# Kernel tuning notes

Measured on AMD Instinct MI355X. Metric: run time of the kernel, lower is better.

The kernel has to match this reference:

```python
import jax, jax.numpy as jnp
import numpy as np

BN_EPS = 1e-5


def setup_inputs() -> dict:
    key = jax.random.key(0)
    ks = jax.random.split(key, 12)
    B, C, L, P = 8, 128, 4096, 96
    d = C // 8
    return {
        "x": jax.random.normal(ks[0], (B, C, 1), jnp.float32),
        "Wt": jax.random.normal(ks[1], (C, C, L), jnp.float32) * 0.02,
        "bt": jax.random.normal(ks[2], (C,), jnp.float32) * 0.02,
        "gamma": jnp.ones((C,), jnp.float32),
        "beta": jnp.zeros((C,), jnp.float32),
        "Wq": jax.random.normal(ks[3], (d, C), jnp.float32) * 0.05,
        "bq": jax.random.normal(ks[4], (d,), jnp.float32) * 0.02,
        "Wk": jax.random.normal(ks[5], (d, C), jnp.float32) * 0.05,
        "bk": jax.random.normal(ks[6], (d,), jnp.float32) * 0.02,
        "Wv": jax.random.normal(ks[7], (C, C), jnp.float32) * 0.05,
        "bv": jax.random.normal(ks[8], (C,), jnp.float32) * 0.02,
        "W2": jax.random.normal(ks[9], (P, C), jnp.float32) * 0.05,
        "b2": jax.random.normal(ks[10], (P,), jnp.float32) * 0.02,
    }


def reference(x, Wt, bt, gamma, beta, Wq, bq, Wk, bk, Wv, bv, W2, b2):
    # l1: ConvTranspose1d(C, C, kernel=L, stride=1) on input of length 1
    # out[b, o, l] = sum_i x[b, i, 0] * Wt[i, o, l] + bt[o]
    h = jnp.einsum('bi,iol->bol', x[:, :, 0], Wt) + bt[None, :, None]  # [B,C,L]
    # BatchNorm1d (training mode: batch stats, biased variance)
    mean = jnp.mean(h, axis=(0, 2), keepdims=True)
    var = jnp.mean((h - mean) ** 2, axis=(0, 2), keepdims=True)
    h = (h - mean) * jax.lax.rsqrt(var + BN_EPS)
    h = h * gamma[None, :, None] + beta[None, :, None]
    h = jax.nn.relu(h)
    # Self_Attn: 1x1 conv projections
    q = jnp.einsum('qc,bcl->bql', Wq, h) + bq[None, :, None]   # [B,d,L]
    k = jnp.einsum('qc,bcl->bql', Wk, h) + bk[None, :, None]   # [B,d,L]
    v = jnp.einsum('oc,bcl->bol', Wv, h) + bv[None, :, None]   # [B,C,L]
    energy = jnp.einsum('bdl,bdm->blm', q, k)                  # [B,L,L]
    attn = jax.nn.softmax(energy, axis=-1)
    out = jnp.einsum('bcm,blm->bcl', v, attn)                  # [B,C,L]
    # l2: Conv1d(C -> P, kernel=1)
    y = jnp.einsum('pc,bcl->bpl', W2, out) + b2[None, :, None]  # [B,P,L]
    return y
```

## Files before the change

### kernel.cpp

```cpp
#include <hip/hip_runtime.h>

#define B_ 8
#define C_ 128
#define L_ 4096
#define P_ 96
#define D_ 16

typedef __attribute__((ext_vector_type(8))) short short8;
typedef __attribute__((ext_vector_type(16))) float float16v;

__device__ __forceinline__ unsigned short f2bf(float f) {
  unsigned int u = __float_as_uint(f);
  u += 0x7fff + ((u >> 16) & 1);
  return (unsigned short)(u >> 16);
}

constexpr size_t OFF_H      = 0;
constexpr size_t OFF_PSUM   = 16777216;
constexpr size_t OFF_PSUMSQ = OFF_PSUM + 8192;
constexpr size_t OFF_SCALE  = OFF_PSUMSQ + 8192;
constexpr size_t OFF_SHIFT  = OFF_SCALE + 512;
constexpr size_t OFF_WALLT  = OFF_SHIFT + 512;
constexpr size_t OFF_BALL   = OFF_WALLT + 65536;
constexpr size_t OFF_QT     = OFF_BALL + 512;
constexpr size_t OFF_KT     = OFF_QT + 1048576;
constexpr size_t OFF_V2     = OFF_KT + 1048576;

__global__ __launch_bounds__(128) void k_prep(
    const float* __restrict__ Wq, const float* __restrict__ bq,
    const float* __restrict__ Wk, const float* __restrict__ bk,
    const float* __restrict__ Wv, const float* __restrict__ bv,
    const float* __restrict__ W2,
    float* __restrict__ wallT, float* __restrict__ ball)
{
  const int r = blockIdx.x;
  const int c = threadIdx.x;
  float wv;
  if (r < 16) {
    wv = Wq[r * C_ + c];
  } else if (r < 32) {
    wv = Wk[(r - 16) * C_ + c];
  } else {
    const int p = r - 32;
    float s = 0.f;
#pragma unroll 8
    for (int o = 0; o < C_; ++o) s += W2[p * C_ + o] * Wv[o * C_ + c];
    wv = s;
  }
  wallT[c * C_ + r] = wv;
  if (c == 0) {
    float bb;
    if (r < 16)      bb = bq[r];
    else if (r < 32) bb = bk[r - 16];
    else {
      const int p = r - 32;
      float s = 0.f;
#pragma unroll 8
      for (int o = 0; o < C_; ++o) s += W2[p * C_ + o] * bv[o];
      bb = s;
    }
    ball[r] = bb;
  }
}

__global__ __launch_bounds__(512) void k_conv(
    const float* __restrict__ x, const float* __restrict__ Wt,
    float* __restrict__ h, float* __restrict__ psum, float* __restrict__ psumsq)
{
  __shared__ float4 xs4[256];
  __shared__ float rs1[8], rs2[8];
  const int tid = threadIdx.x;
  const int o = blockIdx.y;
  const int l = blockIdx.x * 2048 + tid * 4;

  if (tid < 256) xs4[tid] = ((const float4*)x)[tid];
  __syncthreads();

  float4 acc[8];
#pragma unroll
  for (int bb = 0; bb < 8; ++bb) acc[bb] = (float4){0.f, 0.f, 0.f, 0.f};

  const float* wp = Wt + (size_t)o * L_ + l;
  const size_t stride = (size_t)C_ * L_;
  const int phase = (blockIdx.y + blockIdx.x * 8) & 31;

  float4 wbuf[2][4];
#pragma unroll
  for (int q = 0; q < 4; ++q)
    wbuf[0][q] = *(const float4*)(wp + (size_t)(phase * 4 + q) * stride);

#pragma unroll 2
  for (int g = 0; g < 32; ++g) {
    const int cur = g & 1, nb = cur ^ 1;
    const int in4 = ((phase + g + 1) & 31) * 4;
#pragma unroll
    for (int q = 0; q < 4; ++q)
      wbuf[nb][q] = *(const float4*)(wp + (size_t)(in4 + q) * stride);

    const int ic = (phase + g) & 31;
#pragma unroll
    for (int bb = 0; bb < 8; ++bb) {
      const float4 xb = xs4[bb * 32 + ic];
      acc[bb].x += xb.x * wbuf[cur][0].x + xb.y * wbuf[cur][1].x + xb.z * wbuf[cur][2].x + xb.w * wbuf[cur][3].x;
      acc[bb].y += xb.x * wbuf[cur][0].y + xb.y * wbuf[cur][1].y + xb.z * wbuf[cur][2].y + xb.w * wbuf[cur][3].y;
      acc[bb].z += xb.x * wbuf[cur][0].z + xb.y * wbuf[cur][1].z + xb.z * wbuf[cur][2].z + xb.w * wbuf[cur][3].z;
      acc[bb].w += xb.x * wbuf[cur][0].w + xb.y * wbuf[cur][1].w + xb.z * wbuf[cur][2].w + xb.w * wbuf[cur][3].w;
    }
  }
  float s1 = 0.f, s2 = 0.f;
#pragma unroll
  for (int bb = 0; bb < 8; ++bb) {
    *(float4*)(h + ((size_t)(bb * C_ + o)) * L_ + l) = acc[bb];
    s1 += acc[bb].x + acc[bb].y + acc[bb].z + acc[bb].w;
    s2 += acc[bb].x * acc[bb].x + acc[bb].y * acc[bb].y
        + acc[bb].z * acc[bb].z + acc[bb].w * acc[bb].w;
  }
  for (int off = 1; off < 64; off <<= 1) {
    s1 += __shfl_xor(s1, off);
    s2 += __shfl_xor(s2, off);
  }
  if ((tid & 63) == 0) { rs1[tid >> 6] = s1; rs2[tid >> 6] = s2; }
  __syncthreads();
  if (tid == 0) {
    float a1 = 0.f, a2 = 0.f;
#pragma unroll
    for (int wv = 0; wv < 8; ++wv) { a1 += rs1[wv]; a2 += rs2[wv]; }
    psum[o * 2 + blockIdx.x]   = a1;
    psumsq[o * 2 + blockIdx.x] = a2;
  }
}

__global__ __launch_bounds__(128) void k_bn(
    const float* __restrict__ psum, const float* __restrict__ psumsq,
    const float* __restrict__ gamma, const float* __restrict__ beta,
    float* __restrict__ scale, float* __restrict__ shift)
{
  const int c = threadIdx.x;
  float s1 = 0.f, s2 = 0.f;
  for (int t = 0; t < 2; ++t) { s1 += psum[c * 2 + t]; s2 += psumsq[c * 2 + t]; }
  const float inv = 1.f / 32768.f;
  const float mean = s1 * inv;
  const float var  = s2 * inv - mean * mean;
  const float sc   = rsqrtf(var + 1e-5f) * gamma[c];
  scale[c] = sc;
  shift[c] = beta[c] - mean * sc;
}

__global__ __launch_bounds__(256) void k_proj(
    const float* __restrict__ h, const float* __restrict__ scale,
    const float* __restrict__ shift, const float* __restrict__ wallT,
    const float* __restrict__ ball,
    unsigned short* __restrict__ qT, unsigned short* __restrict__ kT,
    unsigned short* __restrict__ v2t)
{
  __shared__ __align__(16) char sm[128 * 68 * 4];
  float* hn = (float*)sm;
  unsigned short* v2s = (unsigned short*)sm;

  const int b = blockIdx.y;
  const int l0 = blockIdx.x * 64;
  const int tid = threadIdx.x;

#pragma unroll
  for (int i = 0; i < 8; ++i) {
    const int idx = tid + i * 256;
    const int c = idx >> 4, lq = (idx & 15) * 4;
    const float4 hv = *(const float4*)(h + ((size_t)(b * C_ + c)) * L_ + l0 + lq);
    const float sc = scale[c], sh = shift[c];
    float4 r;
    r.x = fmaxf(hv.x * sc + sh, 0.f);
    r.y = fmaxf(hv.y * sc + sh, 0.f);
    r.z = fmaxf(hv.z * sc + sh, 0.f);
    r.w = fmaxf(hv.w * sc + sh, 0.f);
    *(float4*)(hn + c * 68 + lq) = r;
  }
  __syncthreads();

  const int wu = __builtin_amdgcn_readfirstlane(tid) >> 6;
  const int lane = tid & 63;
  const int l = l0 + lane;

  float acc[32];
#pragma unroll
  for (int r = 0; r < 32; ++r) acc[r] = ball[wu * 32 + r];

#pragma unroll 4
  for (int c = 0; c < C_; ++c) {
    const float hv = hn[c * 68 + lane];
    const float* wrow = wallT + c * C_ + wu * 32;
#pragma unroll
    for (int r = 0; r < 32; ++r) acc[r] += wrow[r] * hv;
  }
  __syncthreads();

  if (wu == 0) {
    const size_t row = (size_t)(b * L_ + l) * D_;
    short8 v0, v1;
#pragma unroll
    for (int r = 0; r < 8; ++r) {
      v0[r] = (short)f2bf(acc[r] * 1.44269504f);
      v1[r] = (short)f2bf(acc[8 + r] * 1.44269504f);
    }
    *(short8*)(qT + row) = v0;  *(short8*)(qT + row + 8) = v1;
#pragma unroll
    for (int r = 0; r < 8; ++r) { v0[r] = (short)f2bf(acc[16 + r]); v1[r] = (short)f2bf(acc[24 + r]); }
    *(short8*)(kT + row) = v0;  *(short8*)(kT + row + 8) = v1;
  } else {
    const int pbase = wu * 32 - 32;
#pragma unroll
    for (int r = 0; r < 32; ++r)
      v2s[(pbase + r) * 72 + lane] = f2bf(acc[r]);
  }
  __syncthreads();

#pragma unroll
  for (int i = 0; i < 6; ++i) {
    const int j = tid + i * 256;
    const int mo4 = j & 3;
    const int jp = j >> 2;
    const int p = jp % 96;
    const int mtl = jp / 96;
    const uint2 val = *(const uint2*)(v2s + p * 72 + mtl * 16 + mo4 * 4);
    *(uint2*)(v2t + ((size_t)((b * (L_ / 16) + blockIdx.x * 4 + mtl)) * P_ + p) * 16
              + mo4 * 4) = val;
  }
}

__global__ __launch_bounds__(1024, 4) void k_attn(
    const unsigned short* __restrict__ qT, const unsigned short* __restrict__ kT,
    const unsigned short* __restrict__ v2t, const float* __restrict__ b2,
    float* __restrict__ y)
{
  __shared__ float ldsO[P_ * 128];
  __shared__ float ldsL[128];

  const int b = blockIdx.y;
  const int l0 = blockIdx.x * 128;
  const int tid = threadIdx.x;
  const int w  = tid >> 6;
  const int qg = w & 3;
  const int ms = w >> 2;
  const int lane = tid & 63;
  const int col = lane & 31;
  const int hh  = lane >> 5;

#pragma unroll
  for (int i = 0; i < 12; ++i) ldsO[tid + i * 1024] = 0.f;
  if (tid < 128) ldsL[tid] = 0.f;
  __syncthreads();

  const int lq = l0 + qg * 32 + col;
  const short8 qf = *(const short8*)(qT + ((size_t)(b * L_ + lq)) * D_ + hh * 8);

  float16v oacc[3];
#pragma unroll
  for (int pt = 0; pt < 3; ++pt)
#pragma unroll
    for (int r = 0; r < 16; ++r) oacc[pt][r] = 0.f;
  float lsum = 0.f;

  const unsigned short* kbase =
      kT + ((size_t)(b * L_ + ms * 1024 + col)) * D_ + hh * 8;
  const unsigned short* vtb = v2t + (size_t)b * (L_ / 16) * P_ * 16
                              + (size_t)col * 16 + hh * 8;

  short8 kf_cur = *(const short8*)(kbase);

#pragma unroll 2
  for (int it = 0; it < 32; ++it) {
    const int itn = (it + 1) & 31;
    const short8 kf_nxt = *(const short8*)(kbase + (size_t)itn * 32 * D_);

    float16v zero;
#pragma unroll
    for (int r = 0; r < 16; ++r) zero[r] = 0.f;
    const float16v s = __builtin_amdgcn_mfma_f32_32x32x16_bf16(kf_cur, qf, zero, 0, 0, 0);

    const int mt16 = ms * 64 + it * 2;

#pragma unroll
    for (int mt = 0; mt < 2; ++mt) {
      short8 vf[3];
#pragma unroll
      for (int pt = 0; pt < 3; ++pt)
        vf[pt] = *(const short8*)(vtb + ((size_t)(mt16 + mt) * P_ + pt * 32) * 16);

      unsigned dw[4];
#pragma unroll
      for (int g = 0; g < 4; ++g) {
        const float e0 = __builtin_amdgcn_exp2f(s[8 * mt + 2 * g]);
        const float e1 = __builtin_amdgcn_exp2f(s[8 * mt + 2 * g + 1]);
        lsum += e0 + e1;
        const unsigned u0 = __float_as_uint(e0) + 0x8000u;
        const unsigned u1 = __float_as_uint(e1) + 0x8000u;
        dw[g] = __builtin_amdgcn_perm(u1, u0, 0x07060302u);
      }

      const unsigned t0 = hh ? dw[0] : dw[2];
      const unsigned t1 = hh ? dw[1] : dw[3];
      const unsigned r0 = (unsigned)__shfl_xor((int)t0, 32);
      const unsigned r1 = (unsigned)__shfl_xor((int)t1, 32);
      union { int4 i; short8 s8; } pu;
      pu.i.x = hh ? (int)r0 : (int)dw[0];
      pu.i.y = hh ? (int)r1 : (int)dw[1];
      pu.i.z = hh ? (int)dw[2] : (int)r0;
      pu.i.w = hh ? (int)dw[3] : (int)r1;
      const short8 pf = pu.s8;
#pragma unroll
      for (int pt = 0; pt < 3; ++pt)
        oacc[pt] = __builtin_amdgcn_mfma_f32_32x32x16_bf16(vf[pt], pf, oacc[pt], 0, 0, 0);
    }
    kf_cur = kf_nxt;
  }

  atomicAdd(&ldsL[qg * 32 + col], lsum);
#pragma unroll
  for (int pt = 0; pt < 3; ++pt)
#pragma unroll
    for (int r = 0; r < 16; ++r) {
      const int p = (r & 3) + 8 * (r >> 2) + 4 * hh + 32 * pt;
      atomicAdd(&ldsO[p * 128 + qg * 32 + col], oacc[pt][r]);
    }
  __syncthreads();

#pragma unroll
  for (int i = 0; i < 12; ++i) {
    const int idx = tid + i * 1024;
    const int p = idx >> 7;
    const int l = idx & 127;
    y[((size_t)(b * P_ + p)) * L_ + l0 + l] = ldsO[idx] / ldsL[l] + b2[p];
  }
}

extern "C" void kernel_launch(void* const* d_in, const int* in_sizes, int n_in,
                              void* d_out, int out_size, void* d_ws, size_t ws_size,
                              hipStream_t stream) {
  (void)in_sizes; (void)n_in; (void)out_size; (void)ws_size;
  const float* x     = (const float*)d_in[0];
  const float* Wt    = (const float*)d_in[1];
  const float* gamma = (const float*)d_in[3];
  const float* beta  = (const float*)d_in[4];
  const float* Wq    = (const float*)d_in[5];
  const float* bq    = (const float*)d_in[6];
  const float* Wk    = (const float*)d_in[7];
  const float* bk    = (const float*)d_in[8];
  const float* Wv    = (const float*)d_in[9];
  const float* bv    = (const float*)d_in[10];
  const float* W2    = (const float*)d_in[11];
  const float* b2    = (const float*)d_in[12];
  float* y = (float*)d_out;

  char* ws = (char*)d_ws;
  float* h       = (float*)(ws + OFF_H);
  float* psum    = (float*)(ws + OFF_PSUM);
  float* psumsq  = (float*)(ws + OFF_PSUMSQ);
  float* scale   = (float*)(ws + OFF_SCALE);
  float* shift   = (float*)(ws + OFF_SHIFT);
  float* wallT   = (float*)(ws + OFF_WALLT);
  float* ball    = (float*)(ws + OFF_BALL);
  unsigned short* qT  = (unsigned short*)(ws + OFF_QT);
  unsigned short* kT  = (unsigned short*)(ws + OFF_KT);
  unsigned short* v2t = (unsigned short*)(ws + OFF_V2);

  k_prep<<<128, 128, 0, stream>>>(Wq, bq, Wk, bk, Wv, bv, W2, wallT, ball);
  k_conv<<<dim3(2, 128), 512, 0, stream>>>(x, Wt, h, psum, psumsq);
  k_bn<<<1, 128, 0, stream>>>(psum, psumsq, gamma, beta, scale, shift);
  k_proj<<<dim3(64, 8), 256, 0, stream>>>(h, scale, shift, wallT, ball, qT, kT, v2t);
  k_attn<<<dim3(32, 8), 1024, 0, stream>>>(qT, kT, v2t, b2, y);
}
```

Baseline: 526.0 us.

## Fuse all stages into one cooperative persistent kernel with grid syncs

Replaces the five separate launches (weight prep, transposed conv with BN stats, BN finalize, projections, attention) with one cooperative kernel of 256 blocks of 512 threads. Grid-wide syncs separate the stages, and each block recomputes the BN scale and shift locally. The aim is to remove launch gaps and inter-kernel drains. The trade-off is that the attention stage now runs with 512 threads per block and splits keys two ways instead of using 1024-thread blocks, which may reduce latency hiding. The old launch path is kept as a fallback if the cooperative launch fails.

```diff
diff --git a/kernel.cpp b/kernel.cpp
--- a/kernel.cpp
+++ b/kernel.cpp
@@ -1,4 +1,7 @@
 #include <hip/hip_runtime.h>
+#include <hip/hip_cooperative_groups.h>
+
+namespace cg = cooperative_groups;
 
 #define B_ 8
 #define C_ 128
@@ -25,6 +28,320 @@
 constexpr size_t OFF_QT     = OFF_BALL + 512;
 constexpr size_t OFF_KT     = OFF_QT + 1048576;
 constexpr size_t OFF_V2     = OFF_KT + 1048576;
+
+__global__ __launch_bounds__(512, 2) void k_fused(
+    const float* __restrict__ x, const float* __restrict__ Wt,
+    const float* __restrict__ gamma, const float* __restrict__ beta,
+    const float* __restrict__ Wq, const float* __restrict__ bq,
+    const float* __restrict__ Wk, const float* __restrict__ bk,
+    const float* __restrict__ Wv, const float* __restrict__ bv,
+    const float* __restrict__ W2, const float* __restrict__ b2,
+    float* __restrict__ y,
+    float* __restrict__ h, float* __restrict__ psum, float* __restrict__ psumsq,
+    float* __restrict__ wallT, float* __restrict__ ball,
+    unsigned short* __restrict__ qT, unsigned short* __restrict__ kT,
+    unsigned short* __restrict__ v2t)
+{
+  cg::grid_group grid = cg::this_grid();
+
+  __shared__ __align__(16) char smem[50688];
+  float4* xs4      = (float4*)smem;
+  float*  rs1      = (float*)(smem + 4096);
+  float*  rs2      = (float*)(smem + 4160);
+  float*  ls_scale = (float*)(smem + 49664);
+  float*  ls_shift = (float*)(smem + 50176);
+
+  const int bid = blockIdx.x;
+  const int tid = threadIdx.x;
+
+  if (tid < 64) {
+    const int r = bid >> 1;
+    const int c = (bid & 1) * 64 + tid;
+    float wv;
+    if (r < 16) {
+      wv = Wq[r * C_ + c];
+    } else if (r < 32) {
+      wv = Wk[(r - 16) * C_ + c];
+    } else {
+      const int p = r - 32;
+      float s = 0.f;
+#pragma unroll 8
+      for (int o = 0; o < C_; ++o) s += W2[p * C_ + o] * Wv[o * C_ + c];
+      wv = s;
+    }
+    wallT[c * C_ + r] = wv;
+    if (c == 0) {
+      float bb;
+      if (r < 16)      bb = bq[r];
+      else if (r < 32) bb = bk[r - 16];
+      else {
+        const int p = r - 32;
+        float s = 0.f;
+#pragma unroll 8
+        for (int o = 0; o < C_; ++o) s += W2[p * C_ + o] * bv[o];
+        bb = s;
+      }
+      ball[r] = bb;
+    }
+  }
+
+  {
+    const int o  = bid >> 1;
+    const int lt = bid & 1;
+    const int l  = lt * 2048 + tid * 4;
+
+    if (tid < 256) xs4[tid] = ((const float4*)x)[tid];
+    __syncthreads();
+
+    float4 acc[8];
+#pragma unroll
+    for (int bb = 0; bb < 8; ++bb) acc[bb] = (float4){0.f, 0.f, 0.f, 0.f};
+
+    const float* wp = Wt + (size_t)o * L_ + l;
+    const size_t stride = (size_t)C_ * L_;
+    const int phase = (o + lt * 8) & 31;
+
+    float4 wbuf[2][4];
+#pragma unroll
+    for (int q = 0; q < 4; ++q)
+      wbuf[0][q] = *(const float4*)(wp + (size_t)(phase * 4 + q) * stride);
+
+#pragma unroll 2
+    for (int g = 0; g < 32; ++g) {
+      const int cur = g & 1, nb = cur ^ 1;
+      const int in4 = ((phase + g + 1) & 31) * 4;
+#pragma unroll
+      for (int q = 0; q < 4; ++q)
+        wbuf[nb][q] = *(const float4*)(wp + (size_t)(in4 + q) * stride);
+
+      const int ic = (phase + g) & 31;
+#pragma unroll
+      for (int bb = 0; bb < 8; ++bb) {
+        const float4 xb = xs4[bb * 32 + ic];
+        acc[bb].x += xb.x * wbuf[cur][0].x + xb.y * wbuf[cur][1].x + xb.z * wbuf[cur][2].x + xb.w * wbuf[cur][3].x;
+        acc[bb].y += xb.x * wbuf[cur][0].y + xb.y * wbuf[cur][1].y + xb.z * wbuf[cur][2].y + xb.w * wbuf[cur][3].y;
+        acc[bb].z += xb.x * wbuf[cur][0].z + xb.y * wbuf[cur][1].z + xb.z * wbuf[cur][2].z + xb.w * wbuf[cur][3].z;
+        acc[bb].w += xb.x * wbuf[cur][0].w + xb.y * wbuf[cur][1].w + xb.z * wbuf[cur][2].w + xb.w * wbuf[cur][3].w;
+      }
+    }
+    float s1 = 0.f, s2 = 0.f;
+#pragma unroll
+    for (int bb = 0; bb < 8; ++bb) {
+      *(float4*)(h + ((size_t)(bb * C_ + o)) * L_ + l) = acc[bb];
+      s1 += acc[bb].x + acc[bb].y + acc[bb].z + acc[bb].w;
+      s2 += acc[bb].x * acc[bb].x + acc[bb].y * acc[bb].y
+          + acc[bb].z * acc[bb].z + acc[bb].w * acc[bb].w;
+    }
+    for (int off = 1; off < 64; off <<= 1) {
+      s1 += __shfl_xor(s1, off);
+      s2 += __shfl_xor(s2, off);
+    }
+    if ((tid & 63) == 0) { rs1[tid >> 6] = s1; rs2[tid >> 6] = s2; }
+    __syncthreads();
+    if (tid == 0) {
+      float a1 = 0.f, a2 = 0.f;
+#pragma unroll
+      for (int wv = 0; wv < 8; ++wv) { a1 += rs1[wv]; a2 += rs2[wv]; }
+      psum[o * 2 + lt]   = a1;
+      psumsq[o * 2 + lt] = a2;
+    }
+  }
+
+  grid.sync();
+
+  if (tid < 128) {
+    const float s1 = psum[tid * 2] + psum[tid * 2 + 1];
+    const float s2 = psumsq[tid * 2] + psumsq[tid * 2 + 1];
+    const float inv = 1.f / 32768.f;
+    const float mean = s1 * inv;
+    const float var  = s2 * inv - mean * mean;
+    const float sc   = rsqrtf(var + 1e-5f) * gamma[tid];
+    ls_scale[tid] = sc;
+    ls_shift[tid] = beta[tid] - mean * sc;
+  }
+  __syncthreads();
+
+  for (int jj = 0; jj < 2; ++jj) {
+    const int job = bid * 2 + jj;
+    const int bb_ = job >> 6;
+    const int lx  = job & 63;
+    const int l0  = lx * 64;
+    float* hn = (float*)smem;
+    unsigned short* v2s = (unsigned short*)smem;
+
+#pragma unroll
+    for (int i = 0; i < 4; ++i) {
+      const int idx = tid + i * 512;
+      const int c = idx >> 4, lq = (idx & 15) * 4;
+      const float4 hv = *(const float4*)(h + ((size_t)(bb_ * C_ + c)) * L_ + l0 + lq);
+      const float sc = ls_scale[c], sh = ls_shift[c];
+      float4 r;
+      r.x = fmaxf(hv.x * sc + sh, 0.f);
+      r.y = fmaxf(hv.y * sc + sh, 0.f);
+      r.z = fmaxf(hv.z * sc + sh, 0.f);
+      r.w = fmaxf(hv.w * sc + sh, 0.f);
+      *(float4*)(hn + c * 68 + lq) = r;
+    }
+    __syncthreads();
+
+    const int wu = __builtin_amdgcn_readfirstlane(tid) >> 6;
+    const int lane = tid & 63;
+    const int l = l0 + lane;
+    const int rb = wu * 16;
+
+    float acc[16];
+#pragma unroll
+    for (int r = 0; r < 16; ++r) acc[r] = ball[rb + r];
+
+#pragma unroll 4
+    for (int c = 0; c < C_; ++c) {
+      const float hv = hn[c * 68 + lane];
+      const float* wrow = wallT + c * C_ + rb;
+#pragma unroll
+      for (int r = 0; r < 16; ++r) acc[r] += wrow[r] * hv;
+    }
+    __syncthreads();
+
+    if (wu == 0) {
+      const size_t row = (size_t)(bb_ * L_ + l) * D_;
+      short8 v0, v1;
+#pragma unroll
+      for (int r = 0; r < 8; ++r) {
+        v0[r] = (short)f2bf(acc[r] * 1.44269504f);
+        v1[r] = (short)f2bf(acc[8 + r] * 1.44269504f);
+      }
+      *(short8*)(qT + row) = v0;  *(short8*)(qT + row + 8) = v1;
+    } else if (wu == 1) {
+      const size_t row = (size_t)(bb_ * L_ + l) * D_;
+      short8 v0, v1;
+#pragma unroll
+      for (int r = 0; r < 8; ++r) { v0[r] = (short)f2bf(acc[r]); v1[r] = (short)f2bf(acc[8 + r]); }
+      *(short8*)(kT + row) = v0;  *(short8*)(kT + row + 8) = v1;
+    } else {
+      const int pbase = rb - 32;
+#pragma unroll
+      for (int r = 0; r < 16; ++r)
+        v2s[(pbase + r) * 72 + lane] = f2bf(acc[r]);
+    }
+    __syncthreads();
+
+#pragma unroll
+    for (int i = 0; i < 3; ++i) {
+      const int j = tid + i * 512;
+      const int mo4 = j & 3;
+      const int jp = j >> 2;
+      const int p = jp % 96;
+      const int mtl = jp / 96;
+      const uint2 val = *(const uint2*)(v2s + p * 72 + mtl * 16 + mo4 * 4);
+      *(uint2*)(v2t + ((size_t)((bb_ * (L_ / 16) + lx * 4 + mtl)) * P_ + p) * 16
+                + mo4 * 4) = val;
+    }
+    __syncthreads();
+  }
+
+  grid.sync();
+
+  {
+    const int b  = bid >> 5;
+    const int l0 = (bid & 31) * 128;
+    float* ldsO = (float*)smem;
+    float* ldsL = (float*)(smem + 49152);
+
+#pragma unroll
+    for (int i = 0; i < 24; ++i) ldsO[tid + i * 512] = 0.f;
+    if (tid < 128) ldsL[tid] = 0.f;
+    __syncthreads();
+
+    const int w    = tid >> 6;
+    const int qg   = w & 3;
+    const int ms   = w >> 2;
+    const int lane = tid & 63;
+    const int col  = lane & 31;
+    const int hh   = lane >> 5;
+
+    const int lq = l0 + qg * 32 + col;
+    const short8 qf = *(const short8*)(qT + ((size_t)(b * L_ + lq)) * D_ + hh * 8);
+
+    float16v oacc[3];
+#pragma unroll
+    for (int pt = 0; pt < 3; ++pt)
+#pragma unroll
+      for (int r = 0; r < 16; ++r) oacc[pt][r] = 0.f;
+    float lsum = 0.f;
+
+    const unsigned short* kbase =
+        kT + ((size_t)(b * L_ + ms * 2048 + col)) * D_ + hh * 8;
+    const unsigned short* vtb = v2t + (size_t)b * (L_ / 16) * P_ * 16
+                                + (size_t)col * 16 + hh * 8;
+
+    short8 kf_cur = *(const short8*)(kbase);
+
+#pragma unroll 2
+    for (int it = 0; it < 64; ++it) {
+      const int itn = (it + 1) & 63;
+      const short8 kf_nxt = *(const short8*)(kbase + (size_t)itn * 32 * D_);
+
+      float16v zero;
+#pragma unroll
+      for (int r = 0; r < 16; ++r) zero[r] = 0.f;
+      const float16v s = __builtin_amdgcn_mfma_f32_32x32x16_bf16(kf_cur, qf, zero, 0, 0, 0);
+
+      const int mt16 = ms * 128 + it * 2;
+
+#pragma unroll
+      for (int mt = 0; mt < 2; ++mt) {
+        short8 vf[3];
+#pragma unroll
+        for (int pt = 0; pt < 3; ++pt)
+          vf[pt] = *(const short8*)(vtb + ((size_t)(mt16 + mt) * P_ + pt * 32) * 16);
+
+        unsigned dw[4];
+#pragma unroll
+        for (int g = 0; g < 4; ++g) {
+          const float e0 = __builtin_amdgcn_exp2f(s[8 * mt + 2 * g]);
+          const float e1 = __builtin_amdgcn_exp2f(s[8 * mt + 2 * g + 1]);
+          lsum += e0 + e1;
+          const unsigned u0 = __float_as_uint(e0) + 0x8000u;
+          const unsigned u1 = __float_as_uint(e1) + 0x8000u;
+          dw[g] = __builtin_amdgcn_perm(u1, u0, 0x07060302u);
+        }
+
+        const unsigned t0 = hh ? dw[0] : dw[2];
+        const unsigned t1 = hh ? dw[1] : dw[3];
+        const unsigned r0 = (unsigned)__shfl_xor((int)t0, 32);
+        const unsigned r1 = (unsigned)__shfl_xor((int)t1, 32);
+        union { int4 i; short8 s8; } pu;
+        pu.i.x = hh ? (int)r0 : (int)dw[0];
+        pu.i.y = hh ? (int)r1 : (int)dw[1];
+        pu.i.z = hh ? (int)dw[2] : (int)r0;
+        pu.i.w = hh ? (int)dw[3] : (int)r1;
+        const short8 pf = pu.s8;
+#pragma unroll
+        for (int pt = 0; pt < 3; ++pt)
+          oacc[pt] = __builtin_amdgcn_mfma_f32_32x32x16_bf16(vf[pt], pf, oacc[pt], 0, 0, 0);
+      }
+      kf_cur = kf_nxt;
+    }
+
+    atomicAdd(&ldsL[qg * 32 + col], lsum);
+#pragma unroll
+    for (int pt = 0; pt < 3; ++pt)
+#pragma unroll
+      for (int r = 0; r < 16; ++r) {
+        const int p = (r & 3) + 8 * (r >> 2) + 4 * hh + 32 * pt;
+        atomicAdd(&ldsO[p * 128 + qg * 32 + col], oacc[pt][r]);
+      }
+    __syncthreads();
+
+#pragma unroll
+    for (int i = 0; i < 24; ++i) {
+      const int idx = tid + i * 512;
+      const int p = idx >> 7;
+      const int l = idx & 127;
+      y[((size_t)(b * P_ + p)) * L_ + l0 + l] = ldsO[idx] / ldsL[l] + b2[p];
+    }
+  }
+}
 
 __global__ __launch_bounds__(128) void k_prep(
     const float* __restrict__ Wq, const float* __restrict__ bq,
@@ -308,7 +625,7 @@
       const short8 pf = pu.s8;
 #pragma unroll
       for (int pt = 0; pt < 3; ++pt)
-        oacc[pt] = __builtin_amdgcn_mfma_f32_32x32x16_bf16(vf[pt], pf, oacc[pt], 0, 0, 0);
+        oacc[pt] = __builtin_amdgcn_mfma_f32_32x32x16_bf16(vf[mt * 0 + pt], pf, oacc[pt], 0, 0, 0);
     }
     kf_cur = kf_nxt;
   }
@@ -362,9 +679,20 @@
   unsigned short* kT  = (unsigned short*)(ws + OFF_KT);
   unsigned short* v2t = (unsigned short*)(ws + OFF_V2);
 
-  k_prep<<<128, 128, 0, stream>>>(Wq, bq, Wk, bk, Wv, bv, W2, wallT, ball);
-  k_conv<<<dim3(2, 128), 512, 0, stream>>>(x, Wt, h, psum, psumsq);
-  k_bn<<<1, 128, 0, stream>>>(psum, psumsq, gamma, beta, scale, shift);
-  k_proj<<<dim3(64, 8), 256, 0, stream>>>(h, scale, shift, wallT, ball, qT, kT, v2t);
-  k_attn<<<dim3(32, 8), 1024, 0, stream>>>(qT, kT, v2t, b2, y);
-}
+  void* kargs[] = {
+      (void*)&x, (void*)&Wt, (void*)&gamma, (void*)&beta,
+      (void*)&Wq, (void*)&bq, (void*)&Wk, (void*)&bk,
+      (void*)&Wv, (void*)&bv, (void*)&W2, (void*)&b2,
+      (void*)&y, (void*)&h, (void*)&psum, (void*)&psumsq,
+      (void*)&wallT, (void*)&ball, (void*)&qT, (void*)&kT, (void*)&v2t};
+  const hipError_t cerr = hipLaunchCooperativeKernel(
+      (const void*)k_fused, dim3(256), dim3(512), kargs, 0, stream);
+
+  if (cerr != hipSuccess) {
+    k_prep<<<128, 128, 0, stream>>>(Wq, bq, Wk, bk, Wv, bv, W2, wallT, ball);
+    k_conv<<<dim3(2, 128), 512, 0, stream>>>(x, Wt, h, psum, psumsq);
+    k_bn<<<1, 128, 0, stream>>>(psum, psumsq, gamma, beta, scale, shift);
+    k_proj<<<dim3(64, 8), 256, 0, stream>>>(h, scale, shift, wallT, ball, qT, kT, v2t);
+    k_attn<<<dim3(32, 8), 1024, 0, stream>>>(qT, kT, v2t, b2, y);
+  }
+}
```

Result: slower. 625.7 us (+18.9%).
